# Performance work log

Measured on AMD Instinct MI355X. Metric: run time of the kernel, lower is better.

## Reference

```python
import jax, jax.numpy as jnp
import numpy as np

NUM_STEPS = 8
ADD_IDENTITY = True
EPS = 1e-12
STANDARDIZE = True


def setup_inputs() -> dict:
    key = jax.random.key(0)
    N = 4096
    E = 65536  # avg degree 16
    edge_index = jax.random.randint(key, (2, E), 0, N, dtype=jnp.int64 if jax.config.jax_enable_x64 else jnp.int32)
    edge_weight = jnp.ones((E,), dtype=jnp.float32)
    return {"edge_index": edge_index, "edge_weight": edge_weight, "num_nodes": N}


def reference(edge_index, edge_weight, num_nodes):
    # A[i,j] = sum of edge_weight over edges (row=i, col=j); scipy sums duplicates,
    # and segment_sum does the same.
    row, col = edge_index[0], edge_index[1]
    # deg_j = column sums of A (A.sum(axis=0))
    deg = jax.ops.segment_sum(edge_weight, col, num_segments=num_nodes)
    deg = jnp.maximum(deg, EPS)
    # M = A @ D^{-1}:  M[row, col] = w / deg[col]
    w = edge_weight / deg[col]  # [E]

    # Carry dense propagator P = M^t, extract diagonals for t = 1..NUM_STEPS.
    P0 = jnp.eye(num_nodes, dtype=jnp.float32)  # [N, N]

    def step(P, _):
        # P_new[i, :] = sum_{edges (i=row, j=col)} w_e * P[j, :]
        P = jax.ops.segment_sum(w[:, None] * P[col], row, num_segments=num_nodes)
        return P, jnp.diagonal(P)

    _, diags = jax.lax.scan(step, P0, None, length=NUM_STEPS)  # [T, N]

    X = diags.T  # [N, T]
    if ADD_IDENTITY:
        X = jnp.concatenate([jnp.ones((num_nodes, 1), dtype=jnp.float32), X], axis=1)
    if STANDARDIZE:
        mean = X.mean(axis=0, keepdims=True)
        std = jnp.maximum(X.std(axis=0, keepdims=True), 1e-6)  # ddof=0 == unbiased=False
        X = (X - mean) / std
    return X
```

## Files before the change

kernel.cpp:

```cpp
#include <hip/hip_runtime.h>

#define NN 4096
#define TSTEPS 8
#define EPSW 1e-12f
#define SLABW 512
#define NSLAB 8
#define LSLAB 9
#define BUCKET 64
#define LBUCK 6
#define SLAB_ELEMS ((size_t)NN * SLABW)

typedef unsigned int uint32;
typedef uint32 uint4v __attribute__((ext_vector_type(4)));
typedef float f32x2 __attribute__((ext_vector_type(2)));

__device__ __forceinline__ uint32 bf16rn(float f) {
  uint32 b = __float_as_uint(f);
  return (b + 0x7FFFu + ((b >> 16) & 1u)) >> 16;
}
__device__ __forceinline__ float bf2f(ushort u) {
  return __uint_as_float(((uint32)u) << 16);
}
__device__ __forceinline__ int sphys(int c) {
  int blk = c >> 3;
  return ((blk ^ ((blk >> 3) & 7)) << 3) | (c & 7);
}

__global__ __launch_bounds__(256) void deg_kernel(
    const int* __restrict__ cols, const float* __restrict__ ew,
    float* __restrict__ deg, int E) {
  int e = blockIdx.x * 256 + threadIdx.x;
  if (e >= E) return;
  atomicAdd(deg + cols[e], ew[e]);
}

__global__ __launch_bounds__(256) void scatter_kernel(
    const int* __restrict__ rows, const int* __restrict__ cols,
    const float* __restrict__ ew, const float* __restrict__ deg,
    int* __restrict__ fill, int* __restrict__ col_s, float* __restrict__ w_s,
    int E) {
  int e = blockIdx.x * 256 + threadIdx.x;
  if (e >= E) return;
  int r = rows[e], c = cols[e];
  float w = ew[e] / fmaxf(deg[c], EPSW);
  int pos = atomicAdd(fill + r, 1);
  if (pos < BUCKET) {
    col_s[(r << LBUCK) + pos] = c;
    w_s[(r << LBUCK) + pos] = w;
  }
}

__global__ __launch_bounds__(64) void m2_csr_kernel(
    const int* __restrict__ fill, const int* __restrict__ col_s,
    const float* __restrict__ w_s, ushort* __restrict__ dst,
    float* __restrict__ diags) {
  int i = blockIdx.x;
  int tid = threadIdx.x;
  __shared__ float acc[NN];
  float4 z4 = make_float4(0.f, 0.f, 0.f, 0.f);
#pragma unroll
  for (int k = 0; k < 16; ++k) *(float4*)(acc + k * 256 + tid * 4) = z4;
  int cnt = min(fill[i], BUCKET);
  __syncthreads();
  int myc = 0, fj = 0;
  float myw = 0.f;
  if (tid < cnt) {
    myc = col_s[(i << LBUCK) + tid];
    myw = w_s[(i << LBUCK) + tid];
    fj = min(fill[myc], BUCKET);
  }
  float sl = (tid < cnt && myc == i) ? myw : 0.f;
#pragma unroll
  for (int o = 32; o; o >>= 1) sl += __shfl_down(sl, o);
  if (tid == 0) diags[i] = sl;

  int g = tid >> 4, f0 = tid & 15;
  for (int e = 0; e < cnt; e += 4) {
    int idx = e + g;
    bool v = idx < cnt;
    int srcl = v ? idx : 0;
    int j = __shfl(myc, srcl);
    float we = __shfl(myw, srcl);
    int fc = __shfl(fj, srcl);
    if (v) {
      for (int f = f0; f < fc; f += 16)
        atomicAdd(acc + sphys(col_s[(j << LBUCK) + f]),
                  we * w_s[(j << LBUCK) + f]);
    }
  }
  __syncthreads();
  if (tid == 0) diags[NN + i] = acc[sphys(i)];
#pragma unroll
  for (int p = 0; p < 8; ++p) {
    int c = p * SLABW + tid * 8;
    int ph = sphys(c);
    float4 lo = *(const float4*)(acc + ph);
    float4 hi = *(const float4*)(acc + ph + 4);
    uint4v o;
    o.x = bf16rn(lo.x) | (bf16rn(lo.y) << 16);
    o.y = bf16rn(lo.z) | (bf16rn(lo.w) << 16);
    o.z = bf16rn(hi.x) | (bf16rn(hi.y) << 16);
    o.w = bf16rn(hi.z) | (bf16rn(hi.w) << 16);
    *(uint4v*)(dst + (size_t)p * SLAB_ELEMS + (size_t)i * SLABW + tid * 8) = o;
  }
}

#define FMA8(u, wv)                                          \
  do {                                                       \
    f32x2 w2_ = {(wv), (wv)};                                \
    _Pragma("unroll") for (int q = 0; q < 4; ++q) {          \
      f32x2 p_;                                              \
      p_.x = __uint_as_float((u)[q] << 16);                  \
      p_.y = __uint_as_float((u)[q] & 0xFFFF0000u);          \
      acc2[q] = p_ * w2_ + acc2[q];                          \
    }                                                        \
  } while (0)

__global__ __launch_bounds__(256) void spmm_kernel(
    const ushort* __restrict__ src, ushort* __restrict__ dst,
    const int* __restrict__ fill, const int* __restrict__ col_s,
    const float* __restrict__ w_s, float* __restrict__ diags, int tIdx) {
  int b = blockIdx.x;
  int slab = b & (NSLAB - 1);
  int wv = threadIdx.x >> 6;
  int lane = threadIdx.x & 63;
  int i = ((b >> 3) << 2) | wv;
  int cnt = min(fill[i], BUCKET);
  __shared__ int sc_all[4][64];
  __shared__ float sw_all[4][64];
  int* sc = sc_all[wv];
  float* sw = sw_all[wv];
  f32x2 acc2[4];
#pragma unroll
  for (int q = 0; q < 4; ++q) acc2[q] = (f32x2){0.f, 0.f};
  const ushort* sbase = src + (size_t)slab * SLAB_ELEMS + lane * 8;

  if (lane < cnt) {
    sc[lane] = col_s[(i << LBUCK) + lane];
    sw[lane] = w_s[(i << LBUCK) + lane];
  }
  int k = 0;
  for (; k + 8 <= cnt; k += 8) {
    uint4v u0 = *(const uint4v*)(sbase + ((size_t)sc[k]     << LSLAB));
    uint4v u1 = *(const uint4v*)(sbase + ((size_t)sc[k + 1] << LSLAB));
    uint4v u2 = *(const uint4v*)(sbase + ((size_t)sc[k + 2] << LSLAB));
    uint4v u3 = *(const uint4v*)(sbase + ((size_t)sc[k + 3] << LSLAB));
    uint4v u4 = *(const uint4v*)(sbase + ((size_t)sc[k + 4] << LSLAB));
    uint4v u5 = *(const uint4v*)(sbase + ((size_t)sc[k + 5] << LSLAB));
    uint4v u6 = *(const uint4v*)(sbase + ((size_t)sc[k + 6] << LSLAB));
    uint4v u7 = *(const uint4v*)(sbase + ((size_t)sc[k + 7] << LSLAB));
    float w0 = sw[k], w1 = sw[k + 1], w2 = sw[k + 2], w3 = sw[k + 3];
    float w4 = sw[k + 4], w5 = sw[k + 5], w6 = sw[k + 6], w7 = sw[k + 7];
    FMA8(u0, w0); FMA8(u1, w1); FMA8(u2, w2); FMA8(u3, w3);
    FMA8(u4, w4); FMA8(u5, w5); FMA8(u6, w6); FMA8(u7, w7);
  }
  for (; k + 4 <= cnt; k += 4) {
    uint4v u0 = *(const uint4v*)(sbase + ((size_t)sc[k]     << LSLAB));
    uint4v u1 = *(const uint4v*)(sbase + ((size_t)sc[k + 1] << LSLAB));
    uint4v u2 = *(const uint4v*)(sbase + ((size_t)sc[k + 2] << LSLAB));
    uint4v u3 = *(const uint4v*)(sbase + ((size_t)sc[k + 3] << LSLAB));
    float w0 = sw[k], w1 = sw[k + 1], w2 = sw[k + 2], w3 = sw[k + 3];
    FMA8(u0, w0); FMA8(u1, w1); FMA8(u2, w2); FMA8(u3, w3);
  }
  for (; k < cnt; ++k) {
    uint4v u = *(const uint4v*)(sbase + ((size_t)sc[k] << LSLAB));
    float w = sw[k];
    FMA8(u, w);
  }

  uint4v o;
#pragma unroll
  for (int q = 0; q < 4; ++q)
    o[q] = bf16rn(acc2[q].x) | (bf16rn(acc2[q].y) << 16);
  *(uint4v*)(dst + (size_t)slab * SLAB_ELEMS + (size_t)i * SLABW + lane * 8) = o;

  if ((i >> LSLAB) == slab) {
    int lc = i & (SLABW - 1);
    if ((lc >> 3) == lane) {
      int m = lc & 7;
      f32x2 pr = acc2[m >> 1];
      float v = (m & 1) ? pr.y : pr.x;
      diags[tIdx * NN + i] = v;
    }
  }
}

__device__ __forceinline__ size_t slab_addr(int row, int col) {
  return ((size_t)(col >> LSLAB)) * SLAB_ELEMS + (size_t)row * SLABW + (col & (SLABW - 1));
}
__device__ __forceinline__ float elem8(uint4v lo, uint4v hi, int c) {
  uint32 u = (c < 8) ? lo[(c & 7) >> 1] : hi[(c & 7) >> 1];
  return __uint_as_float((c & 1) ? (u & 0xFFFF0000u) : (u << 16));
}

__global__ __launch_bounds__(256) void trace_kernel(
    const ushort* __restrict__ M2, const ushort* __restrict__ M3,
    const ushort* __restrict__ M4, float* __restrict__ part) {
  int bid = blockIdx.x;
  int bi = bid >> 3, jc = bid & 7;
  int tid = threadIdx.x;
  __shared__ ushort b3[64 * 64], b4[64 * 64];
  __shared__ float red[4][4][64];
  int lr = tid >> 2, lc0 = (tid & 3) * 16;
  int r = tid & 63, jq = tid >> 6;
  float s5 = 0.f, s6 = 0.f, s7 = 0.f, s8 = 0.f;

  for (int it = 0; it < 8; ++it) {
    int bj = jc * 8 + it;
    {
      int gj = bj * 64 + lr;
      int gc = bi * 64 + lc0;
      size_t base = slab_addr(gj, gc);
      uint4v v3a = *(const uint4v*)(M3 + base);
      uint4v v3b = *(const uint4v*)(M3 + base + 8);
      uint4v v4a = *(const uint4v*)(M4 + base);
      uint4v v4b = *(const uint4v*)(M4 + base + 8);
      int cb0 = (lc0 >> 3) ^ (lr & 7);
      int cb1 = ((lc0 >> 3) + 1) ^ (lr & 7);
      *(uint4v*)(b3 + lr * 64 + cb0 * 8) = v3a;
      *(uint4v*)(b3 + lr * 64 + cb1 * 8) = v3b;
      *(uint4v*)(b4 + lr * 64 + cb0 * 8) = v4a;
      *(uint4v*)(b4 + lr * 64 + cb1 * 8) = v4b;
    }
    __syncthreads();
    int gi = bi * 64 + r;
    int gc0 = bj * 64 + jq * 16;
    size_t abase = slab_addr(gi, gc0);
    uint4v a2a = *(const uint4v*)(M2 + abase);
    uint4v a2b = *(const uint4v*)(M2 + abase + 8);
    uint4v a3a = *(const uint4v*)(M3 + abase);
    uint4v a3b = *(const uint4v*)(M3 + abase + 8);
    uint4v a4a = *(const uint4v*)(M4 + abase);
    uint4v a4b = *(const uint4v*)(M4 + abase + 8);
#pragma unroll
    for (int c = 0; c < 16; ++c) {
      int jj = jq * 16 + c;
      int idx = jj * 64 + ((((r >> 3) ^ (jj & 7)) << 3) | (r & 7));
      float bv3 = bf2f(b3[idx]);
      float bv4 = bf2f(b4[idx]);
      float av2 = elem8(a2a, a2b, c);
      float av3 = elem8(a3a, a3b, c);
      float av4 = elem8(a4a, a4b, c);
      s5 += av2 * bv3;
      s6 += av3 * bv3;
      s7 += av3 * bv4;
      s8 += av4 * bv4;
    }
    __syncthreads();
  }
  red[0][jq][r] = s5;
  red[1][jq][r] = s6;
  red[2][jq][r] = s7;
  red[3][jq][r] = s8;
  __syncthreads();
  if (tid < 64) {
    int gi = bi * 64 + tid;
#pragma unroll
    for (int v = 0; v < 4; ++v) {
      float s = red[v][0][tid] + red[v][1][tid] + red[v][2][tid] + red[v][3][tid];
      part[((size_t)v * 8 + jc) * NN + gi] = s;
    }
  }
}

__global__ __launch_bounds__(256) void finalize_kernel(
    const float* __restrict__ diags, const float* __restrict__ part,
    float* __restrict__ out) {
  int k = blockIdx.x;
  int tid = threadIdx.x;
  float vals[16];
  float sum = 0.f, sq = 0.f;
#pragma unroll
  for (int j = 0; j < 16; ++j) {
    int i = j * 256 + tid;
    float v;
    if (k == 0) {
      v = 1.0f;
    } else if (k <= 4) {
      v = diags[(size_t)(k - 1) * NN + i];
    } else {
      v = 0.f;
      const float* p = part + (size_t)(k - 5) * 8 * NN + i;
#pragma unroll
      for (int jc = 0; jc < 8; ++jc) v += p[(size_t)jc * NN];
    }
    vals[j] = v;
    sum += v;
    sq += v * v;
  }
#pragma unroll
  for (int off = 32; off; off >>= 1) {
    sum += __shfl_down(sum, off);
    sq += __shfl_down(sq, off);
  }
  __shared__ float s0[4], s1[4];
  __shared__ float smean, sinv;
  int wid = tid >> 6, lane = tid & 63;
  if (lane == 0) { s0[wid] = sum; s1[wid] = sq; }
  __syncthreads();
  if (tid == 0) {
    float S = s0[0] + s0[1] + s0[2] + s0[3];
    float Q = s1[0] + s1[1] + s1[2] + s1[3];
    float mean = S / (float)NN;
    float var = Q / (float)NN - mean * mean;
    var = fmaxf(var, 0.f);
    float sd = fmaxf(sqrtf(var), 1e-6f);
    smean = mean;
    sinv = 1.f / sd;
  }
  __syncthreads();
#pragma unroll
  for (int j = 0; j < 16; ++j) {
    int i = j * 256 + tid;
    out[i * (TSTEPS + 1) + k] = (vals[j] - smean) * sinv;
  }
}

extern "C" void kernel_launch(void* const* d_in, const int* in_sizes, int n_in,
                              void* d_out, int out_size, void* d_ws, size_t ws_size,
                              hipStream_t stream) {
  const int* ei = (const int*)d_in[0];
  const float* ew = (const float*)d_in[1];
  int E = in_sizes[1];
  const int* rows = ei;
  const int* cols = ei + E;

  char* ws = (char*)d_ws;
  size_t off = 0;
  auto alloc = [&](size_t bytes) {
    void* p = ws + off;
    off = (off + bytes + 255) & ~(size_t)255;
    return p;
  };
  float* deg   = (float*)alloc(NN * 4);
  int*   fill  = (int*)alloc(NN * 4);
  size_t zbytes = off;
  float* diags = (float*)alloc((size_t)4 * NN * 4);
  float* part  = (float*)alloc((size_t)4 * 8 * NN * 4);
  int*   col_s = (int*)alloc((size_t)NN * BUCKET * 4);
  float* w_s   = (float*)alloc((size_t)NN * BUCKET * 4);
  ushort* bufA = (ushort*)alloc((size_t)NN * NN * 2);
  ushort* bufB = (ushort*)alloc((size_t)NN * NN * 2);
  ushort* bufC = (ushort*)alloc((size_t)NN * NN * 2);

  hipMemsetAsync(deg, 0, zbytes, stream);

  int eb = (E + 255) / 256;
  deg_kernel<<<eb, 256, 0, stream>>>(cols, ew, deg, E);
  scatter_kernel<<<eb, 256, 0, stream>>>(rows, cols, ew, deg, fill, col_s, w_s, E);

  m2_csr_kernel<<<NN, 64, 0, stream>>>(fill, col_s, w_s, bufA, diags);
  spmm_kernel<<<(NN / 4) * NSLAB, 256, 0, stream>>>(bufA, bufB, fill, col_s, w_s, diags, 2);
  spmm_kernel<<<(NN / 4) * NSLAB, 256, 0, stream>>>(bufB, bufC, fill, col_s, w_s, diags, 3);
  trace_kernel<<<512, 256, 0, stream>>>(bufA, bufB, bufC, part);

  finalize_kernel<<<TSTEPS + 1, 256, 0, stream>>>(diags, part, (float*)d_out);
}
```

Before: 133.9 us.

## Narrow SpMM column slabs to 128 so each lane loads one bf16 pair

```diff
diff --git a/kernel.cpp b/kernel.cpp
--- a/kernel.cpp
+++ b/kernel.cpp
@@ -3,9 +3,9 @@
 #define NN 4096
 #define TSTEPS 8
 #define EPSW 1e-12f
-#define SLABW 512
-#define NSLAB 8
-#define LSLAB 9
+#define SLABW 128
+#define NSLAB 32
+#define LSLAB 7
 #define BUCKET 64
 #define LBUCK 6
 #define SLAB_ELEMS ((size_t)NN * SLABW)
@@ -92,7 +92,7 @@
   if (tid == 0) diags[NN + i] = acc[sphys(i)];
 #pragma unroll
   for (int p = 0; p < 8; ++p) {
-    int c = p * SLABW + tid * 8;
+    int c = p * 512 + tid * 8;
     int ph = sphys(c);
     float4 lo = *(const float4*)(acc + ph);
     float4 hi = *(const float4*)(acc + ph + 4);
@@ -101,19 +101,18 @@
     o.y = bf16rn(lo.z) | (bf16rn(lo.w) << 16);
     o.z = bf16rn(hi.x) | (bf16rn(hi.y) << 16);
     o.w = bf16rn(hi.z) | (bf16rn(hi.w) << 16);
-    *(uint4v*)(dst + (size_t)p * SLAB_ELEMS + (size_t)i * SLABW + tid * 8) = o;
-  }
-}
-
-#define FMA8(u, wv)                                          \
+    *(uint4v*)(dst + (size_t)(c >> LSLAB) * SLAB_ELEMS + (size_t)i * SLABW +
+               (c & (SLABW - 1))) = o;
+  }
+}
+
+#define FMA1(u, wv)                                          \
   do {                                                       \
     f32x2 w2_ = {(wv), (wv)};                                \
-    _Pragma("unroll") for (int q = 0; q < 4; ++q) {          \
-      f32x2 p_;                                              \
-      p_.x = __uint_as_float((u)[q] << 16);                  \
-      p_.y = __uint_as_float((u)[q] & 0xFFFF0000u);          \
-      acc2[q] = p_ * w2_ + acc2[q];                          \
-    }                                                        \
+    f32x2 p_;                                                \
+    p_.x = __uint_as_float((u) << 16);                       \
+    p_.y = __uint_as_float((u) & 0xFFFF0000u);               \
+    acc2 = p_ * w2_ + acc2;                                  \
   } while (0)
 
 __global__ __launch_bounds__(256) void spmm_kernel(
@@ -121,19 +120,18 @@
     const int* __restrict__ fill, const int* __restrict__ col_s,
     const float* __restrict__ w_s, float* __restrict__ diags, int tIdx) {
   int b = blockIdx.x;
-  int slab = b & (NSLAB - 1);
+  int phase = b >> 13;
+  int slab = (phase << 3) | (b & 7);
   int wv = threadIdx.x >> 6;
   int lane = threadIdx.x & 63;
-  int i = ((b >> 3) << 2) | wv;
+  int i = (((b >> 3) & 1023) << 2) | wv;
   int cnt = min(fill[i], BUCKET);
   __shared__ int sc_all[4][64];
   __shared__ float sw_all[4][64];
   int* sc = sc_all[wv];
   float* sw = sw_all[wv];
-  f32x2 acc2[4];
-#pragma unroll
-  for (int q = 0; q < 4; ++q) acc2[q] = (f32x2){0.f, 0.f};
-  const ushort* sbase = src + (size_t)slab * SLAB_ELEMS + lane * 8;
+  f32x2 acc2 = {0.f, 0.f};
+  const ushort* sbase = src + (size_t)slab * SLAB_ELEMS + lane * 2;
 
   if (lane < cnt) {
     sc[lane] = col_s[(i << LBUCK) + lane];
@@ -141,46 +139,40 @@
   }
   int k = 0;
   for (; k + 8 <= cnt; k += 8) {
-    uint4v u0 = *(const uint4v*)(sbase + ((size_t)sc[k]     << LSLAB));
-    uint4v u1 = *(const uint4v*)(sbase + ((size_t)sc[k + 1] << LSLAB));
-    uint4v u2 = *(const uint4v*)(sbase + ((size_t)sc[k + 2] << LSLAB));
-    uint4v u3 = *(const uint4v*)(sbase + ((size_t)sc[k + 3] << LSLAB));
-    uint4v u4 = *(const uint4v*)(sbase + ((size_t)sc[k + 4] << LSLAB));
-    uint4v u5 = *(const uint4v*)(sbase + ((size_t)sc[k + 5] << LSLAB));
-    uint4v u6 = *(const uint4v*)(sbase + ((size_t)sc[k + 6] << LSLAB));
-    uint4v u7 = *(const uint4v*)(sbase + ((size_t)sc[k + 7] << LSLAB));
+    uint32 u0 = *(const uint32*)(sbase + (sc[k]     << LSLAB));
+    uint32 u1 = *(const uint32*)(sbase + (sc[k + 1] << LSLAB));
+    uint32 u2 = *(const uint32*)(sbase + (sc[k + 2] << LSLAB));
+    uint32 u3 = *(const uint32*)(sbase + (sc[k + 3] << LSLAB));
+    uint32 u4 = *(const uint32*)(sbase + (sc[k + 4] << LSLAB));
+    uint32 u5 = *(const uint32*)(sbase + (sc[k + 5] << LSLAB));
+    uint32 u6 = *(const uint32*)(sbase + (sc[k + 6] << LSLAB));
+    uint32 u7 = *(const uint32*)(sbase + (sc[k + 7] << LSLAB));
     float w0 = sw[k], w1 = sw[k + 1], w2 = sw[k + 2], w3 = sw[k + 3];
     float w4 = sw[k + 4], w5 = sw[k + 5], w6 = sw[k + 6], w7 = sw[k + 7];
-    FMA8(u0, w0); FMA8(u1, w1); FMA8(u2, w2); FMA8(u3, w3);
-    FMA8(u4, w4); FMA8(u5, w5); FMA8(u6, w6); FMA8(u7, w7);
+    FMA1(u0, w0); FMA1(u1, w1); FMA1(u2, w2); FMA1(u3, w3);
+    FMA1(u4, w4); FMA1(u5, w5); FMA1(u6, w6); FMA1(u7, w7);
   }
   for (; k + 4 <= cnt; k += 4) {
-    uint4v u0 = *(const uint4v*)(sbase + ((size_t)sc[k]     << LSLAB));
-    uint4v u1 = *(const uint4v*)(sbase + ((size_t)sc[k + 1] << LSLAB));
-    uint4v u2 = *(const uint4v*)(sbase + ((size_t)sc[k + 2] << LSLAB));
-    uint4v u3 = *(const uint4v*)(sbase + ((size_t)sc[k + 3] << LSLAB));
+    uint32 u0 = *(const uint32*)(sbase + (sc[k]     << LSLAB));
+    uint32 u1 = *(const uint32*)(sbase + (sc[k + 1] << LSLAB));
+    uint32 u2 = *(const uint32*)(sbase + (sc[k + 2] << LSLAB));
+    uint32 u3 = *(const uint32*)(sbase + (sc[k + 3] << LSLAB));
     float w0 = sw[k], w1 = sw[k + 1], w2 = sw[k + 2], w3 = sw[k + 3];
-    FMA8(u0, w0); FMA8(u1, w1); FMA8(u2, w2); FMA8(u3, w3);
+    FMA1(u0, w0); FMA1(u1, w1); FMA1(u2, w2); FMA1(u3, w3);
   }
   for (; k < cnt; ++k) {
-    uint4v u = *(const uint4v*)(sbase + ((size_t)sc[k] << LSLAB));
+    uint32 u = *(const uint32*)(sbase + (sc[k] << LSLAB));
     float w = sw[k];
-    FMA8(u, w);
-  }
-
-  uint4v o;
-#pragma unroll
-  for (int q = 0; q < 4; ++q)
-    o[q] = bf16rn(acc2[q].x) | (bf16rn(acc2[q].y) << 16);
-  *(uint4v*)(dst + (size_t)slab * SLAB_ELEMS + (size_t)i * SLABW + lane * 8) = o;
+    FMA1(u, w);
+  }
+
+  uint32 o = bf16rn(acc2.x) | (bf16rn(acc2.y) << 16);
+  *(uint32*)(dst + (size_t)slab * SLAB_ELEMS + (size_t)i * SLABW + lane * 2) = o;
 
   if ((i >> LSLAB) == slab) {
     int lc = i & (SLABW - 1);
-    if ((lc >> 3) == lane) {
-      int m = lc & 7;
-      f32x2 pr = acc2[m >> 1];
-      float v = (m & 1) ? pr.y : pr.x;
-      diags[tIdx * NN + i] = v;
+    if ((lc >> 1) == lane) {
+      diags[tIdx * NN + i] = (lc & 1) ? acc2.y : acc2.x;
     }
   }
 }
```

Measured after the change: 161.1 us. 1.2x slower.

## Fuse graph build into cooperative kernel and finalize into trace via last-block

Applied to the files above, without the earlier changes.

```diff
diff --git a/kernel.cpp b/kernel.cpp
--- a/kernel.cpp
+++ b/kernel.cpp
@@ -1,4 +1,7 @@
 #include <hip/hip_runtime.h>
+#include <hip/hip_cooperative_groups.h>
+
+namespace cg = cooperative_groups;
 
 #define NN 4096
 #define TSTEPS 8
@@ -26,27 +29,30 @@
   return ((blk ^ ((blk >> 3) & 7)) << 3) | (c & 7);
 }
 
-__global__ __launch_bounds__(256) void deg_kernel(
-    const int* __restrict__ cols, const float* __restrict__ ew,
-    float* __restrict__ deg, int E) {
-  int e = blockIdx.x * 256 + threadIdx.x;
-  if (e >= E) return;
-  atomicAdd(deg + cols[e], ew[e]);
-}
-
-__global__ __launch_bounds__(256) void scatter_kernel(
+__global__ __launch_bounds__(256) void build_coop(
     const int* __restrict__ rows, const int* __restrict__ cols,
-    const float* __restrict__ ew, const float* __restrict__ deg,
+    const float* __restrict__ ew, float* __restrict__ deg,
     int* __restrict__ fill, int* __restrict__ col_s, float* __restrict__ w_s,
-    int E) {
-  int e = blockIdx.x * 256 + threadIdx.x;
-  if (e >= E) return;
-  int r = rows[e], c = cols[e];
-  float w = ew[e] / fmaxf(deg[c], EPSW);
-  int pos = atomicAdd(fill + r, 1);
-  if (pos < BUCKET) {
-    col_s[(r << LBUCK) + pos] = c;
-    w_s[(r << LBUCK) + pos] = w;
+    int* __restrict__ counter, int E) {
+  cg::grid_group grid = cg::this_grid();
+  int tid = blockIdx.x * 256 + threadIdx.x;
+  int nthr = gridDim.x * 256;
+  for (int k = tid; k < NN; k += nthr) {
+    deg[k] = 0.f;
+    fill[k] = 0;
+  }
+  if (tid == 0) *counter = 0;
+  grid.sync();
+  for (int e = tid; e < E; e += nthr) atomicAdd(deg + cols[e], ew[e]);
+  grid.sync();
+  for (int e = tid; e < E; e += nthr) {
+    int r = rows[e], c = cols[e];
+    float w = ew[e] / fmaxf(deg[c], EPSW);
+    int pos = atomicAdd(fill + r, 1);
+    if (pos < BUCKET) {
+      col_s[(r << LBUCK) + pos] = c;
+      w_s[(r << LBUCK) + pos] = w;
+    }
   }
 }
 
@@ -193,9 +199,11 @@
   return __uint_as_float((c & 1) ? (u & 0xFFFF0000u) : (u << 16));
 }
 
-__global__ __launch_bounds__(256) void trace_kernel(
+__global__ __launch_bounds__(256) void trace_fin_kernel(
     const ushort* __restrict__ M2, const ushort* __restrict__ M3,
-    const ushort* __restrict__ M4, float* __restrict__ part) {
+    const ushort* __restrict__ M4, const float* __restrict__ diags,
+    float* __restrict__ part, int* __restrict__ counter,
+    float* __restrict__ out) {
   int bid = blockIdx.x;
   int bi = bid >> 3, jc = bid & 7;
   int tid = threadIdx.x;
@@ -261,58 +269,61 @@
       part[((size_t)v * 8 + jc) * NN + gi] = s;
     }
   }
-}
-
-__global__ __launch_bounds__(256) void finalize_kernel(
-    const float* __restrict__ diags, const float* __restrict__ part,
-    float* __restrict__ out) {
-  int k = blockIdx.x;
-  int tid = threadIdx.x;
-  float vals[16];
-  float sum = 0.f, sq = 0.f;
-#pragma unroll
-  for (int j = 0; j < 16; ++j) {
-    int i = j * 256 + tid;
-    float v;
-    if (k == 0) {
-      v = 1.0f;
-    } else if (k <= 4) {
-      v = diags[(size_t)(k - 1) * NN + i];
-    } else {
-      v = 0.f;
-      const float* p = part + (size_t)(k - 5) * 8 * NN + i;
-#pragma unroll
-      for (int jc = 0; jc < 8; ++jc) v += p[(size_t)jc * NN];
-    }
-    vals[j] = v;
-    sum += v;
-    sq += v * v;
-  }
-#pragma unroll
-  for (int off = 32; off; off >>= 1) {
-    sum += __shfl_down(sum, off);
-    sq += __shfl_down(sq, off);
-  }
+
+  __threadfence();
+  __shared__ int isLast;
+  if (tid == 0) isLast = (atomicAdd(counter, 1) == 511);
+  __syncthreads();
+  if (!isLast) return;
+  __threadfence();
+
   __shared__ float s0[4], s1[4];
   __shared__ float smean, sinv;
   int wid = tid >> 6, lane = tid & 63;
-  if (lane == 0) { s0[wid] = sum; s1[wid] = sq; }
-  __syncthreads();
-  if (tid == 0) {
-    float S = s0[0] + s0[1] + s0[2] + s0[3];
-    float Q = s1[0] + s1[1] + s1[2] + s1[3];
-    float mean = S / (float)NN;
-    float var = Q / (float)NN - mean * mean;
-    var = fmaxf(var, 0.f);
-    float sd = fmaxf(sqrtf(var), 1e-6f);
-    smean = mean;
-    sinv = 1.f / sd;
-  }
-  __syncthreads();
-#pragma unroll
-  for (int j = 0; j < 16; ++j) {
-    int i = j * 256 + tid;
-    out[i * (TSTEPS + 1) + k] = (vals[j] - smean) * sinv;
+  for (int k = 0; k < TSTEPS + 1; ++k) {
+    float vals[16];
+    float sum = 0.f, sq = 0.f;
+#pragma unroll
+    for (int j = 0; j < 16; ++j) {
+      int i = j * 256 + tid;
+      float v;
+      if (k == 0) {
+        v = 1.0f;
+      } else if (k <= 4) {
+        v = diags[(size_t)(k - 1) * NN + i];
+      } else {
+        v = 0.f;
+        const float* p = part + (size_t)(k - 5) * 8 * NN + i;
+#pragma unroll
+        for (int pc = 0; pc < 8; ++pc) v += p[(size_t)pc * NN];
+      }
+      vals[j] = v;
+      sum += v;
+      sq += v * v;
+    }
+#pragma unroll
+    for (int off = 32; off; off >>= 1) {
+      sum += __shfl_down(sum, off);
+      sq += __shfl_down(sq, off);
+    }
+    if (lane == 0) { s0[wid] = sum; s1[wid] = sq; }
+    __syncthreads();
+    if (tid == 0) {
+      float S = s0[0] + s0[1] + s0[2] + s0[3];
+      float Q = s1[0] + s1[1] + s1[2] + s1[3];
+      float mean = S / (float)NN;
+      float var = fmaxf(Q / (float)NN - mean * mean, 0.f);
+      float sd = fmaxf(sqrtf(var), 1e-6f);
+      smean = mean;
+      sinv = 1.f / sd;
+    }
+    __syncthreads();
+#pragma unroll
+    for (int j = 0; j < 16; ++j) {
+      int i = j * 256 + tid;
+      out[i * (TSTEPS + 1) + k] = (vals[j] - smean) * sinv;
+    }
+    __syncthreads();
   }
 }
 
@@ -332,27 +343,26 @@
     off = (off + bytes + 255) & ~(size_t)255;
     return p;
   };
-  float* deg   = (float*)alloc(NN * 4);
-  int*   fill  = (int*)alloc(NN * 4);
-  size_t zbytes = off;
-  float* diags = (float*)alloc((size_t)4 * NN * 4);
-  float* part  = (float*)alloc((size_t)4 * 8 * NN * 4);
-  int*   col_s = (int*)alloc((size_t)NN * BUCKET * 4);
-  float* w_s   = (float*)alloc((size_t)NN * BUCKET * 4);
-  ushort* bufA = (ushort*)alloc((size_t)NN * NN * 2);
-  ushort* bufB = (ushort*)alloc((size_t)NN * NN * 2);
-  ushort* bufC = (ushort*)alloc((size_t)NN * NN * 2);
-
-  hipMemsetAsync(deg, 0, zbytes, stream);
-
-  int eb = (E + 255) / 256;
-  deg_kernel<<<eb, 256, 0, stream>>>(cols, ew, deg, E);
-  scatter_kernel<<<eb, 256, 0, stream>>>(rows, cols, ew, deg, fill, col_s, w_s, E);
+  float* deg     = (float*)alloc(NN * 4);
+  int*   fill    = (int*)alloc(NN * 4);
+  int*   counter = (int*)alloc(256);
+  float* diags   = (float*)alloc((size_t)4 * NN * 4);
+  float* part    = (float*)alloc((size_t)4 * 8 * NN * 4);
+  int*   col_s   = (int*)alloc((size_t)NN * BUCKET * 4);
+  float* w_s     = (float*)alloc((size_t)NN * BUCKET * 4);
+  ushort* bufA   = (ushort*)alloc((size_t)NN * NN * 2);
+  ushort* bufB   = (ushort*)alloc((size_t)NN * NN * 2);
+  ushort* bufC   = (ushort*)alloc((size_t)NN * NN * 2);
+
+  void* args[] = {(void*)&rows, (void*)&cols, (void*)&ew, (void*)&deg,
+                  (void*)&fill, (void*)&col_s, (void*)&w_s, (void*)&counter,
+                  (void*)&E};
+  hipLaunchCooperativeKernel((void*)build_coop, dim3(256), dim3(256), args, 0,
+                             stream);
 
   m2_csr_kernel<<<NN, 64, 0, stream>>>(fill, col_s, w_s, bufA, diags);
   spmm_kernel<<<(NN / 4) * NSLAB, 256, 0, stream>>>(bufA, bufB, fill, col_s, w_s, diags, 2);
   spmm_kernel<<<(NN / 4) * NSLAB, 256, 0, stream>>>(bufB, bufC, fill, col_s, w_s, diags, 3);
-  trace_kernel<<<512, 256, 0, stream>>>(bufA, bufB, bufC, part);
-
-  finalize_kernel<<<TSTEPS + 1, 256, 0, stream>>>(diags, part, (float*)d_out);
-}
+  trace_fin_kernel<<<512, 256, 0, stream>>>(bufA, bufB, bufC, diags, part,
+                                            counter, (float*)d_out);
+}
```

Measured after the change: 253.7 us. 89.5% more time.
